# Performance work log

Measured on AMD Instinct MI355X. Metric: run time of the kernel, lower is better.

## Reference

```python
import jax, jax.numpy as jnp
import numpy as np

TEMP_EPS = 1e-6


def setup_inputs() -> dict:
    key = jax.random.key(0)
    k1, k2, k3 = jax.random.split(key, 3)
    B, V = 128, 128256
    logits = jax.random.normal(k1, (B, V), dtype=jnp.float32)
    temperatures = jax.random.uniform(k2, (B,), dtype=jnp.float32)
    u = jax.random.uniform(k3, (B, V), dtype=jnp.float32)
    return {"logits": logits, "temperatures": temperatures, "u": u}


def reference(logits, temperatures, u):
    # Faithful vectorized version of the per-row loop:
    #   nan_to_num -> temperature scale -> softmax -> multinomial sample,
    # expressed as a single Gumbel-max over the batch (equivalent sampling
    # distribution), with greedy argmax where temp <= 1e-6.
    logits = jnp.nan_to_num(logits)                       # [B, V]
    greedy = jnp.argmax(logits, axis=-1)                  # [B]

    safe_temp = jnp.maximum(temperatures, TEMP_EPS)[:, None]  # [B, 1]
    scaled = logits / safe_temp                           # [B, V]

    # Gumbel-max trick: argmax(scaled + g), g ~ Gumbel(0,1), samples
    # exactly from softmax(scaled) == the multinomial in the original.
    uc = jnp.clip(u, 1e-10, 1.0 - 1e-7)
    gumbel = -jnp.log(-jnp.log(uc))                       # [B, V]
    sampled = jnp.argmax(scaled + gumbel, axis=-1)        # [B]

    use_greedy = temperatures <= TEMP_EPS                 # [B] bool
    return jnp.where(use_greedy, greedy, sampled)
```

## Files before the change

kernel.cpp:

```cpp
#include <hip/hip_runtime.h>
#include <cfloat>
#include <cstdint>


#define TEMP_EPS 1e-6f

static constexpr int V       = 128256;
static constexpr int V4      = V / 4;
static constexpr int SEGS    = 32;
static constexpr int SEG_V4  = V4 / SEGS;
static constexpr int TAIL    = SEG_V4 - 3 * 256;

__device__ __forceinline__ unsigned long long pack_key(float v, int idx) {
    unsigned b = __float_as_uint(v);
    unsigned mask = (unsigned)(((int)b >> 31)) | 0x80000000u;
    b ^= mask;
    return ((unsigned long long)b << 32) | (unsigned)(~(unsigned)idx);
}

__device__ __forceinline__ unsigned long long umax64(unsigned long long a,
                                                     unsigned long long b) {
    return a > b ? a : b;
}

__device__ __forceinline__ float neg_log_fast(float c) {
    float t = c - 1.0f;
    float p = -1.0f / 6.0f;
    p = __builtin_fmaf(p, t, 0.2f);
    p = __builtin_fmaf(p, t, -0.25f);
    p = __builtin_fmaf(p, t, 1.0f / 3.0f);
    p = __builtin_fmaf(p, t, -0.5f);
    p = __builtin_fmaf(p, t, 1.0f);
    float wpoly = -t * p;
    float whw = -__logf(c);
    return (c >= 0.90625f) ? wpoly : whw;
}

__global__ __launch_bounds__(256) void sampler_partial_kernel(
    const float* __restrict__ logits,
    const float* __restrict__ temps,
    const float* __restrict__ u,
    unsigned long long* __restrict__ partials) {
    const int row = blockIdx.y;
    const int seg = blockIdx.x;
    const int tid = threadIdx.x;

    const float temp = temps[row];
    const bool greedy = (temp <= TEMP_EPS);
    const float safe_temp = fmaxf(temp, TEMP_EPS);
    const float inv_temp = 1.0f / safe_temp;

    const float4* __restrict__ l4 = (const float4*)(logits + (size_t)row * V);
    const float4* __restrict__ u4 = (const float4*)(u + (size_t)row * V);

    const float UC_LO = 1e-10f;
    const float UC_HI = (float)(1.0 - 1e-7);

    const int base = seg * SEG_V4;

    int idx[4];
    idx[0] = base + tid;
    idx[1] = base + 256 + tid;
    idx[2] = base + 512 + tid;
    idx[3] = (tid < TAIL) ? (base + 768 + tid) : (base + tid);

    float best_v = -FLT_MAX;
    int   best_i = 0x7FFFFFFF;

    if (greedy) {
        float4 lv[4];
#pragma unroll
        for (int k = 0; k < 4; ++k) lv[k] = l4[idx[k]];
#pragma unroll
        for (int k = 0; k < 4; ++k) {
            const int e = idx[k] * 4;
            float m01 = fmaxf(lv[k].x, lv[k].y);
            float m23 = fmaxf(lv[k].z, lv[k].w);
            float m = fmaxf(m01, m23);
            int ei = (lv[k].x == m) ? e
                   : (lv[k].y == m) ? e + 1
                   : (lv[k].z == m) ? e + 2 : e + 3;
            if (m > best_v) { best_v = m; best_i = ei; }
        }
    } else {
        float4 lv[4], uv[4];
#pragma unroll
        for (int k = 0; k < 4; ++k) {
            lv[k] = l4[idx[k]];
            uv[k] = u4[idx[k]];
        }

#pragma unroll
        for (int k = 0; k < 4; ++k) {
            const int e = idx[k] * 4;

            float c0 = fminf(fmaxf(uv[k].x, UC_LO), UC_HI);
            float c1 = fminf(fmaxf(uv[k].y, UC_LO), UC_HI);
            float c2 = fminf(fmaxf(uv[k].z, UC_LO), UC_HI);
            float c3 = fminf(fmaxf(uv[k].w, UC_LO), UC_HI);

            float w0 = neg_log_fast(c0);
            float w1 = neg_log_fast(c1);
            float w2 = neg_log_fast(c2);
            float w3 = neg_log_fast(c3);

            float g0 = -__logf(w0);
            float g1 = -__logf(w1);
            float g2 = -__logf(w2);
            float g3 = -__logf(w3);

            float v0 = __builtin_fmaf(lv[k].x, inv_temp, g0);
            float v1 = __builtin_fmaf(lv[k].y, inv_temp, g1);
            float v2 = __builtin_fmaf(lv[k].z, inv_temp, g2);
            float v3 = __builtin_fmaf(lv[k].w, inv_temp, g3);

            float m01 = fmaxf(v0, v1);
            float m23 = fmaxf(v2, v3);
            float m = fmaxf(m01, m23);
            int ei = (v0 == m) ? e
                   : (v1 == m) ? e + 1
                   : (v2 == m) ? e + 2 : e + 3;
            if (m > best_v) { best_v = m; best_i = ei; }
        }
    }

    unsigned long long key = pack_key(best_v, best_i);

    for (int o = 32; o > 0; o >>= 1)
        key = umax64(key, __shfl_down(key, o));

    __shared__ unsigned long long sdata[4];
    if ((tid & 63) == 0) sdata[tid >> 6] = key;
    __syncthreads();

    if (tid == 0) {
        for (int w = 1; w < 4; ++w) key = umax64(key, sdata[w]);
        partials[row * SEGS + seg] = key;
    }
}

__global__ __launch_bounds__(64) void sampler_reduce_kernel(
    const unsigned long long* __restrict__ partials,
    int* __restrict__ out) {
    const int row = blockIdx.x;
    const int t = threadIdx.x;
    unsigned long long key = (t < SEGS) ? partials[row * SEGS + t] : 0ULL;
    for (int o = 32; o > 0; o >>= 1)
        key = umax64(key, __shfl_down(key, o));
    if (t == 0)
        out[row] = (int)(~(unsigned)(key & 0xFFFFFFFFull));
}

extern "C" void kernel_launch(void* const* d_in, const int* in_sizes, int n_in,
                              void* d_out, int out_size, void* d_ws, size_t ws_size,
                              hipStream_t stream) {
    const float* logits = (const float*)d_in[0];
    const float* temps  = (const float*)d_in[1];
    const float* u      = (const float*)d_in[2];
    int* out = (int*)d_out;
    const int B = in_sizes[1];

    unsigned long long* partials = (unsigned long long*)d_ws;

    dim3 grid1(SEGS, B);
    hipLaunchKernelGGL(sampler_partial_kernel, grid1, dim3(256), 0, stream,
                       logits, temps, u, partials);
    hipLaunchKernelGGL(sampler_reduce_kernel, dim3(B), dim3(64), 0, stream,
                       partials, out);
}
```

Baseline: 145.5 us.

## Use persistent blocks with double-buffered register prefetch across tasks

Replaces the one-block-per-(row,segment) grid with 512 persistent blocks. Each block handles 8 tasks and issues the loads for the next task while computing the current one, using two register slots. It also drops the shared-memory cross-wave reduction: each wave writes its own partial key, and the reduce kernel now combines 128 partials per row with 128 threads. The aim is to hide memory latency and cut launch and synchronisation overhead, at the cost of doubled register pressure and lower occupancy. The PBLOCKS*PITERS tasks and the 128 partials per row are hardcoded for B=128.

```diff
diff --git a/kernel.cpp b/kernel.cpp
--- a/kernel.cpp
+++ b/kernel.cpp
@@ -10,6 +10,8 @@
 static constexpr int SEGS    = 32;
 static constexpr int SEG_V4  = V4 / SEGS;
 static constexpr int TAIL    = SEG_V4 - 3 * 256;
+static constexpr int PBLOCKS = 512;
+static constexpr int PITERS  = 8;
 
 __device__ __forceinline__ unsigned long long pack_key(float v, int idx) {
     unsigned b = __float_as_uint(v);
@@ -41,114 +43,116 @@
     const float* __restrict__ temps,
     const float* __restrict__ u,
     unsigned long long* __restrict__ partials) {
-    const int row = blockIdx.y;
-    const int seg = blockIdx.x;
-    const int tid = threadIdx.x;
-
-    const float temp = temps[row];
-    const bool greedy = (temp <= TEMP_EPS);
-    const float safe_temp = fmaxf(temp, TEMP_EPS);
-    const float inv_temp = 1.0f / safe_temp;
-
-    const float4* __restrict__ l4 = (const float4*)(logits + (size_t)row * V);
-    const float4* __restrict__ u4 = (const float4*)(u + (size_t)row * V);
+    const int tid  = threadIdx.x;
+    const int wave = tid >> 6;
 
     const float UC_LO = 1e-10f;
     const float UC_HI = (float)(1.0 - 1e-7);
 
-    const int base = seg * SEG_V4;
+    float4 lv[2][4], uv[2][4];
 
-    int idx[4];
-    idx[0] = base + tid;
-    idx[1] = base + 256 + tid;
-    idx[2] = base + 512 + tid;
-    idx[3] = (tid < TAIL) ? (base + 768 + tid) : (base + tid);
+    auto issue = [&](int task, int slot) {
+        const int row = task >> 5;
+        const int seg = task & 31;
+        const float4* __restrict__ l4 = (const float4*)(logits + (size_t)row * V);
+        const float4* __restrict__ u4 = (const float4*)(u + (size_t)row * V);
+        const int base = seg * SEG_V4;
+#pragma unroll
+        for (int k = 0; k < 3; ++k) {
+            lv[slot][k] = l4[base + k * 256 + tid];
+            uv[slot][k] = u4[base + k * 256 + tid];
+        }
+        const int i3 = (tid < TAIL) ? (base + 768 + tid) : (base + tid);
+        lv[slot][3] = l4[i3];
+        uv[slot][3] = u4[i3];
+    };
 
-    float best_v = -FLT_MAX;
-    int   best_i = 0x7FFFFFFF;
+    auto compute = [&](int task, int slot) {
+        const int row = task >> 5;
+        const int seg = task & 31;
+        const float temp = temps[row];
+        const bool greedy = (temp <= TEMP_EPS);
+        const float inv_temp = 1.0f / fmaxf(temp, TEMP_EPS);
+        const int base = seg * SEG_V4;
 
-    if (greedy) {
-        float4 lv[4];
+        int idx[4];
+        idx[0] = base + tid;
+        idx[1] = base + 256 + tid;
+        idx[2] = base + 512 + tid;
+        idx[3] = (tid < TAIL) ? (base + 768 + tid) : (base + tid);
+
+        float best_v = -FLT_MAX;
+        int   best_i = 0x7FFFFFFF;
+
+        if (greedy) {
 #pragma unroll
-        for (int k = 0; k < 4; ++k) lv[k] = l4[idx[k]];
+            for (int k = 0; k < 4; ++k) {
+                const float4 l = lv[slot][k];
+                const int e = idx[k] * 4;
+                float m = fmaxf(fmaxf(l.x, l.y), fmaxf(l.z, l.w));
+                int ei = (l.x == m) ? e
+                       : (l.y == m) ? e + 1
+                       : (l.z == m) ? e + 2 : e + 3;
+                if (m > best_v) { best_v = m; best_i = ei; }
+            }
+        } else {
 #pragma unroll
-        for (int k = 0; k < 4; ++k) {
-            const int e = idx[k] * 4;
-            float m01 = fmaxf(lv[k].x, lv[k].y);
-            float m23 = fmaxf(lv[k].z, lv[k].w);
-            float m = fmaxf(m01, m23);
-            int ei = (lv[k].x == m) ? e
-                   : (lv[k].y == m) ? e + 1
-                   : (lv[k].z == m) ? e + 2 : e + 3;
-            if (m > best_v) { best_v = m; best_i = ei; }
-        }
-    } else {
-        float4 lv[4], uv[4];
-#pragma unroll
-        for (int k = 0; k < 4; ++k) {
-            lv[k] = l4[idx[k]];
-            uv[k] = u4[idx[k]];
+            for (int k = 0; k < 4; ++k) {
+                const float4 l = lv[slot][k];
+                const float4 uu = uv[slot][k];
+                const int e = idx[k] * 4;
+
+                float c0 = fminf(fmaxf(uu.x, UC_LO), UC_HI);
+                float c1 = fminf(fmaxf(uu.y, UC_LO), UC_HI);
+                float c2 = fminf(fmaxf(uu.z, UC_LO), UC_HI);
+                float c3 = fminf(fmaxf(uu.w, UC_LO), UC_HI);
+
+                float g0 = -__logf(neg_log_fast(c0));
+                float g1 = -__logf(neg_log_fast(c1));
+                float g2 = -__logf(neg_log_fast(c2));
+                float g3 = -__logf(neg_log_fast(c3));
+
+                float v0 = __builtin_fmaf(l.x, inv_temp, g0);
+                float v1 = __builtin_fmaf(l.y, inv_temp, g1);
+                float v2 = __builtin_fmaf(l.z, inv_temp, g2);
+                float v3 = __builtin_fmaf(l.w, inv_temp, g3);
+
+                float m = fmaxf(fmaxf(v0, v1), fmaxf(v2, v3));
+                int ei = (v0 == m) ? e
+                       : (v1 == m) ? e + 1
+                       : (v2 == m) ? e + 2 : e + 3;
+                if (m > best_v) { best_v = m; best_i = ei; }
+            }
         }
 
+        unsigned long long key = pack_key(best_v, best_i);
+        for (int o = 32; o > 0; o >>= 1)
+            key = umax64(key, __shfl_down(key, o));
+        if ((tid & 63) == 0)
+            partials[task * 4 + wave] = key;
+    };
+
+    issue((int)blockIdx.x, 0);
 #pragma unroll
-        for (int k = 0; k < 4; ++k) {
-            const int e = idx[k] * 4;
-
-            float c0 = fminf(fmaxf(uv[k].x, UC_LO), UC_HI);
-            float c1 = fminf(fmaxf(uv[k].y, UC_LO), UC_HI);
-            float c2 = fminf(fmaxf(uv[k].z, UC_LO), UC_HI);
-            float c3 = fminf(fmaxf(uv[k].w, UC_LO), UC_HI);
-
-            float w0 = neg_log_fast(c0);
-            float w1 = neg_log_fast(c1);
-            float w2 = neg_log_fast(c2);
-            float w3 = neg_log_fast(c3);
-
-            float g0 = -__logf(w0);
-            float g1 = -__logf(w1);
-            float g2 = -__logf(w2);
-            float g3 = -__logf(w3);
-
-            float v0 = __builtin_fmaf(lv[k].x, inv_temp, g0);
-            float v1 = __builtin_fmaf(lv[k].y, inv_temp, g1);
-            float v2 = __builtin_fmaf(lv[k].z, inv_temp, g2);
-            float v3 = __builtin_fmaf(lv[k].w, inv_temp, g3);
-
-            float m01 = fmaxf(v0, v1);
-            float m23 = fmaxf(v2, v3);
-            float m = fmaxf(m01, m23);
-            int ei = (v0 == m) ? e
-                   : (v1 == m) ? e + 1
-                   : (v2 == m) ? e + 2 : e + 3;
-            if (m > best_v) { best_v = m; best_i = ei; }
-        }
-    }
-
-    unsigned long long key = pack_key(best_v, best_i);
-
-    for (int o = 32; o > 0; o >>= 1)
-        key = umax64(key, __shfl_down(key, o));
-
-    __shared__ unsigned long long sdata[4];
-    if ((tid & 63) == 0) sdata[tid >> 6] = key;
-    __syncthreads();
-
-    if (tid == 0) {
-        for (int w = 1; w < 4; ++w) key = umax64(key, sdata[w]);
-        partials[row * SEGS + seg] = key;
+    for (int i = 0; i < PITERS; ++i) {
+        if (i + 1 < PITERS) issue((int)blockIdx.x + (i + 1) * PBLOCKS, (i + 1) & 1);
+        compute((int)blockIdx.x + i * PBLOCKS, i & 1);
     }
 }
 
-__global__ __launch_bounds__(64) void sampler_reduce_kernel(
+__global__ __launch_bounds__(128) void sampler_reduce_kernel(
     const unsigned long long* __restrict__ partials,
     int* __restrict__ out) {
     const int row = blockIdx.x;
     const int t = threadIdx.x;
-    unsigned long long key = (t < SEGS) ? partials[row * SEGS + t] : 0ULL;
+    unsigned long long key = partials[row * 128 + t];
     for (int o = 32; o > 0; o >>= 1)
         key = umax64(key, __shfl_down(key, o));
+    __shared__ unsigned long long s[2];
+    if ((t & 63) == 0) s[t >> 6] = key;
+    __syncthreads();
     if (t == 0)
-        out[row] = (int)(~(unsigned)(key & 0xFFFFFFFFull));
+        out[row] = (int)(~(unsigned)(umax64(s[0], s[1]) & 0xFFFFFFFFull));
 }
 
 extern "C" void kernel_launch(void* const* d_in, const int* in_sizes, int n_in,
@@ -162,9 +166,8 @@
 
     unsigned long long* partials = (unsigned long long*)d_ws;
 
-    dim3 grid1(SEGS, B);
-    hipLaunchKernelGGL(sampler_partial_kernel, grid1, dim3(256), 0, stream,
+    hipLaunchKernelGGL(sampler_partial_kernel, dim3(PBLOCKS), dim3(256), 0, stream,
                        logits, temps, u, partials);
-    hipLaunchKernelGGL(sampler_reduce_kernel, dim3(B), dim3(64), 0, stream,
+    hipLaunchKernelGGL(sampler_reduce_kernel, dim3(B), dim3(128), 0, stream,
                        partials, out);
 }
```

Result: slower. 149.5 us (+2.8%).
